# Performance work log

Measured on AMD Instinct MI355X. Metric: run time of the kernel, lower is better.

## Reference

```python
import jax, jax.numpy as jnp
import numpy as np

B, T, D, H = 8, 1024, 1024, 16
HD = D // H
SCALE = HD ** -0.5


def setup_inputs() -> dict:
    key = jax.random.key(0)
    ks = jax.random.split(key, 5)
    s = 0.02
    return {
        "hidden_states": jax.random.normal(ks[0], (B, T, D), jnp.float32),
        "Wq": jax.random.normal(ks[1], (D, D), jnp.float32) * s,
        "bq": jnp.zeros((D,), jnp.float32),
        "Wk": jax.random.normal(ks[2], (D, D), jnp.float32) * s,
        "bk": jnp.zeros((D,), jnp.float32),
        "Wv": jax.random.normal(ks[3], (D, D), jnp.float32) * s,
        "bv": jnp.zeros((D,), jnp.float32),
        "Wo": jax.random.normal(ks[4], (D, D), jnp.float32) * s,
        "bo": jnp.zeros((D,), jnp.float32),
    }


def _split_heads(x):
    # [B, T, D] -> [B, H, T, HD]
    return x.reshape(B, T, H, HD).transpose(0, 2, 1, 3)


def reference(hidden_states, Wq, bq, Wk, bk, Wv, bv, Wo, bo):
    q = _split_heads((hidden_states @ Wq + bq) * SCALE)
    k = _split_heads(hidden_states @ Wk + bk)
    v = _split_heads(hidden_states @ Wv + bv)
    # [B, H, T, T] attention scores
    scores = jnp.einsum("bhqd,bhkd->bhqk", q, k)
    probs = jax.nn.softmax(scores, axis=-1)
    attn = jnp.einsum("bhqk,bhkd->bhqd", probs, v)
    attn = attn.transpose(0, 2, 1, 3).reshape(B, T, D)
    return attn @ Wo + bo
```

## Files before the change

kernel.cpp:

```cpp
#include <hip/hip_runtime.h>

typedef unsigned short u16;
typedef __attribute__((ext_vector_type(4))) float f32x4;
typedef __attribute__((ext_vector_type(8))) __bf16 bf16x8;
typedef __attribute__((ext_vector_type(4))) __bf16 bf16x4;
typedef __attribute__((ext_vector_type(4))) unsigned short u16x4;
typedef __attribute__((ext_vector_type(8))) unsigned short u16x8;

static __device__ __forceinline__ u16 f2bf(float f) {
    union { float f; unsigned u; } v; v.f = f;
    unsigned r = v.u + 0x7FFFu + ((v.u >> 16) & 1u);
    return (u16)(r >> 16);
}

static __device__ __forceinline__ float exp2f_fast(float x) {
    float r; asm("v_exp_f32 %0, %1" : "=v"(r) : "v"(x)); return r;
}

static __device__ __forceinline__ void gload16(const u16* g, u16* l) {
    __builtin_amdgcn_global_load_lds(
        (const __attribute__((address_space(1))) unsigned int*)g,
        (__attribute__((address_space(3))) unsigned int*)l, 16, 0, 0);
}

template<int N> static __device__ __forceinline__ void vm_wait() {
    if constexpr (N == 3)      asm volatile("s_waitcnt vmcnt(3)" ::: "memory");
    else if constexpr (N == 2) asm volatile("s_waitcnt vmcnt(2)" ::: "memory");
    else                       asm volatile("s_waitcnt vmcnt(0)" ::: "memory");
}

#define SWZ64(row, ec) (((row) * 64) + ((((ec) ^ ((row) & 7))) << 3))

__global__ __launch_bounds__(256) void k_prep(
    const float* __restrict__ hs, u16* __restrict__ Xb,
    const float* __restrict__ W0, const float* __restrict__ W1,
    const float* __restrict__ W2, const float* __restrict__ W3,
    u16* __restrict__ T0, u16* __restrict__ T1, u16* __restrict__ T2, u16* __restrict__ T3,
    float s0) {
    __shared__ float tile[32][33];
    const int id = blockIdx.x;
    const int tid = threadIdx.x;
    if (id < 8192) {
        size_t i = (size_t)id * 256 + tid;
        float4 v = ((const float4*)hs)[i];
        u16x4 o; o[0] = f2bf(v.x); o[1] = f2bf(v.y); o[2] = f2bf(v.z); o[3] = f2bf(v.w);
        *(u16x4*)(Xb + i * 4) = o;
        return;
    }
    const int wid = id - 8192;
    const int z = wid >> 10, rem = wid & 1023;
    const int n0 = (rem & 31) * 32, k0 = (rem >> 5) * 32;
    const float* W; u16* Tt; float sc;
    switch (z) {
        case 0:  W = W0; Tt = T0; sc = s0;  break;
        case 1:  W = W1; Tt = T1; sc = 1.f; break;
        case 2:  W = W2; Tt = T2; sc = 1.f; break;
        default: W = W3; Tt = T3; sc = 1.f; break;
    }
    int r = tid >> 3, c = (tid & 7) * 4;
    float4 v = *(const float4*)(W + (size_t)(k0 + r) * 1024 + n0 + c);
    tile[r][c] = v.x; tile[r][c + 1] = v.y; tile[r][c + 2] = v.z; tile[r][c + 3] = v.w;
    __syncthreads();
    u16x4 o;
    o[0] = f2bf(tile[c][r] * sc);
    o[1] = f2bf(tile[c + 1][r] * sc);
    o[2] = f2bf(tile[c + 2][r] * sc);
    o[3] = f2bf(tile[c + 3][r] * sc);
    *(u16x4*)(Tt + (size_t)(n0 + r) * 1024 + k0 + c) = o;
}

__global__ __launch_bounds__(512, 4) void k_g128(
    const u16* __restrict__ A, const u16* __restrict__ Bt,
    const float* __restrict__ bias, const float* __restrict__ biasK, float qscale,
    u16* __restrict__ obf, u16* __restrict__ obK, float* __restrict__ of32,
    int ldc, int bias_row, int nblk, int cpx, int mode) {
    constexpr int ASLOT = 256 * 32;
    constexpr int BSLOT = 128 * 32;
    __shared__ u16 As[3 * ASLOT];
    __shared__ u16 Bs[3 * BSLOT];
    const int tid = threadIdx.x;
    const int l = tid & 63, w = tid >> 6;
    const int mw = w >> 1, nw = w & 1;
    const int fr = l & 15, gg = l >> 4, f4 = gg * 4;
    const int id = blockIdx.x;
    const int swz = (id & 7) * cpx + (id >> 3);
    const int bm = swz / nblk, bn = swz % nblk;
    const size_t m0 = (size_t)bm * 256, n0v = (size_t)bn * 128;

    const int srow = w * 16 + (l >> 2);
    const int schk = ((l & 3) ^ ((l >> 3) & 3)) * 8;
    const u16* agp0 = A + (m0 + srow) * 1024 + schk;
    const u16* agp1 = A + (m0 + 128 + srow) * 1024 + schk;
    const u16* bgp0 = Bt + (n0v + srow) * 1024 + schk;
    const int ldst = w * 512 + l * 8;

    const int fchk = (gg ^ ((fr >> 1) & 3)) * 8;
    int aoff[4], boff[4];
#pragma unroll
    for (int mt = 0; mt < 4; ++mt) aoff[mt] = (mw * 64 + mt * 16 + fr) * 32 + fchk;
#pragma unroll
    for (int nt = 0; nt < 4; ++nt) boff[nt] = (nw * 64 + nt * 16 + fr) * 32 + fchk;

    f32x4 acc[4][4] = {};

#define GSTG(S, J)                                                              \
    gload16(agp0 + (size_t)(J) * 32, As + (S) * ASLOT + ldst);                  \
    gload16(agp1 + (size_t)(J) * 32, As + (S) * ASLOT + 4096 + ldst);           \
    gload16(bgp0 + (size_t)(J) * 32, Bs + (S) * BSLOT + ldst);
    GSTG(0, 0) GSTG(1, 1)

#define TILE(S, SD, J, VMN, STG)                                                \
    {                                                                           \
        vm_wait<VMN>();                                                         \
        __builtin_amdgcn_s_barrier();                                           \
        bf16x8 afr[4], bfr[4];                                                  \
        _Pragma("unroll")                                                       \
        for (int nt = 0; nt < 4; ++nt)                                          \
            bfr[nt] = *(const bf16x8*)(&Bs[(S) * BSLOT + boff[nt]]);            \
        _Pragma("unroll")                                                       \
        for (int mt = 0; mt < 4; ++mt)                                          \
            afr[mt] = *(const bf16x8*)(&As[(S) * ASLOT + aoff[mt]]);            \
        if (STG) { GSTG(SD, (J) + 2) }                                          \
        __builtin_amdgcn_s_barrier();                                           \
        asm volatile("s_waitcnt lgkmcnt(0)" ::: "memory");                      \
        __builtin_amdgcn_sched_barrier(0);                                      \
        __builtin_amdgcn_s_setprio(1);                                          \
        _Pragma("unroll")                                                       \
        for (int mt = 0; mt < 4; ++mt)                                          \
            _Pragma("unroll")                                                   \
            for (int nt = 0; nt < 4; ++nt)                                      \
                acc[mt][nt] = __builtin_amdgcn_mfma_f32_16x16x32_bf16(afr[mt], bfr[nt], acc[mt][nt], 0, 0, 0); \
        __builtin_amdgcn_s_setprio(0);                                          \
    }

#pragma unroll 1
    for (int jb = 0; jb < 30; jb += 3) {
        TILE(0, 2, jb + 0, 3, true)
        TILE(1, 0, jb + 1, 3, true)
        TILE(2, 1, jb + 2, 3, true)
    }
    TILE(0, 2, 30, 3, false)
    TILE(1, 0, 31, 0, false)
#undef TILE
#undef GSTG

    const int mrow0 = (int)m0 + mw * 64;
    const int ncol0 = (int)n0v + nw * 64;
    if (mode == 1) {
#pragma unroll
        for (int mt = 0; mt < 4; ++mt)
#pragma unroll
            for (int nt = 0; nt < 4; ++nt) {
                const int col = ncol0 + nt * 16 + fr;
                const int seg = col >> 10, colm = col & 1023;
                const float bb = (seg ? biasK[colm] : bias[colm] * qscale);
                u16* op = seg ? obK : obf;
#pragma unroll
                for (int r = 0; r < 4; ++r)
                    op[(size_t)(mrow0 + mt * 16 + f4 + r) * 1024 + colm] = f2bf(acc[mt][nt][r] + bb);
            }
    } else if (mode == 2) {
#pragma unroll
        for (int mt = 0; mt < 4; ++mt) {
            float rb_[4];
#pragma unroll
            for (int r = 0; r < 4; ++r) rb_[r] = bias[mrow0 + mt * 16 + f4 + r];
#pragma unroll
            for (int nt = 0; nt < 4; ++nt) {
                const int col = ncol0 + nt * 16 + fr;
                const int colp = (col & ~31) | (((col >> 2) & 3) << 3) |
                                 (((col >> 4) & 1) << 2) | (col & 3);
#pragma unroll
                for (int r = 0; r < 4; ++r) {
                    const size_t row = (size_t)(mrow0 + mt * 16 + f4 + r);
                    obf[row * (size_t)ldc + colp] = f2bf(acc[mt][nt][r] + rb_[r]);
                }
            }
        }
    } else {
#pragma unroll
        for (int mt = 0; mt < 4; ++mt) {
            float rb_[4];
#pragma unroll
            for (int r = 0; r < 4; ++r)
                rb_[r] = bias_row ? bias[mrow0 + mt * 16 + f4 + r] : 0.f;
#pragma unroll
            for (int nt = 0; nt < 4; ++nt) {
                const int col = ncol0 + nt * 16 + fr;
                const float cb = bias_row ? 0.f : bias[col];
#pragma unroll
                for (int r = 0; r < 4; ++r) {
                    const size_t row = (size_t)(mrow0 + mt * 16 + f4 + r);
                    const float vv = acc[mt][nt][r] + cb + rb_[r];
                    if (of32) of32[row * (size_t)ldc + col] = vv;
                    else      obf[row * (size_t)ldc + col] = f2bf(vv);
                }
            }
        }
    }
}

static __device__ __forceinline__ void qk_tile(const u16* Ks, int fr, int gg,
                                               bf16x8 qA0, bf16x8 qA1, bf16x8 qB0, bf16x8 qB1,
                                               float mA, float mB, f32x4 sA[4], f32x4 sB[4]) {
    __builtin_amdgcn_s_setprio(1);
#pragma unroll
    for (int nt = 0; nt < 4; ++nt) {
        const int rk = nt * 16 + fr;
        const bf16x8 kf0 = *(const bf16x8*)(&Ks[SWZ64(rk, gg)]);
        const bf16x8 kf1 = *(const bf16x8*)(&Ks[SWZ64(rk, gg + 4)]);
        f32x4 z = {-mA, -mA, -mA, -mA};
        z = __builtin_amdgcn_mfma_f32_16x16x32_bf16(kf0, qA0, z, 0, 0, 0);
        z = __builtin_amdgcn_mfma_f32_16x16x32_bf16(kf1, qA1, z, 0, 0, 0);
        sA[nt] = z;
        f32x4 y = {-mB, -mB, -mB, -mB};
        y = __builtin_amdgcn_mfma_f32_16x16x32_bf16(kf0, qB0, y, 0, 0, 0);
        y = __builtin_amdgcn_mfma_f32_16x16x32_bf16(kf1, qB1, y, 0, 0, 0);
        sB[nt] = y;
    }
    __builtin_amdgcn_s_setprio(0);
}

static __device__ __forceinline__ void sm_tile(const f32x4 s[4], f32x4 o[4],
                                               float& m, float& lsum, bf16x4 p[4]) {
    float mymax = s[0][0];
#pragma unroll
    for (int nt = 0; nt < 4; ++nt)
#pragma unroll
        for (int r = 0; r < 4; ++r) mymax = fmaxf(mymax, s[nt][r]);
    float psn[4] = {0.f, 0.f, 0.f, 0.f};
#pragma unroll
    for (int nt = 0; nt < 4; ++nt)
#pragma unroll
        for (int r = 0; r < 4; ++r) {
            const float pp = exp2f_fast(s[nt][r]);
            psn[nt] += pp; p[nt][r] = (__bf16)pp;
        }
    float ps = (psn[0] + psn[1]) + (psn[2] + psn[3]);
    if (__builtin_expect(__any(mymax > 11.0f), 0)) {
        float rm = fmaxf(mymax, __shfl_xor(mymax, 16, 64));
        rm = fmaxf(rm, __shfl_xor(rm, 32, 64));
        const float d = fmaxf(rm, 0.f);
        const float fac = exp2f_fast(-d);
        m += d; lsum *= fac;
#pragma unroll
        for (int mt = 0; mt < 4; ++mt)
#pragma unroll
            for (int r = 0; r < 4; ++r) o[mt][r] *= fac;
        ps = 0.f;
#pragma unroll
        for (int nt = 0; nt < 4; ++nt)
#pragma unroll
            for (int r = 0; r < 4; ++r) {
                const float pp = exp2f_fast(s[nt][r] - d);
                ps += pp; p[nt][r] = (__bf16)pp;
            }
    }
    lsum += ps;
}

static __device__ __forceinline__ void pv_tile(const u16* Vs, int fr, int gg,
                                               const bf16x4 pA[4], const bf16x4 pB[4],
                                               f32x4 oA[4], f32x4 oB[4]) {
    const bf16x8 BA0 = __builtin_shufflevector(pA[0], pA[1], 0, 1, 2, 3, 4, 5, 6, 7);
    const bf16x8 BA1 = __builtin_shufflevector(pA[2], pA[3], 0, 1, 2, 3, 4, 5, 6, 7);
    const bf16x8 BB0 = __builtin_shufflevector(pB[0], pB[1], 0, 1, 2, 3, 4, 5, 6, 7);
    const bf16x8 BB1 = __builtin_shufflevector(pB[2], pB[3], 0, 1, 2, 3, 4, 5, 6, 7);
    __builtin_amdgcn_s_setprio(1);
#pragma unroll
    for (int mt = 0; mt < 4; ++mt) {
        const int rv = mt * 16 + fr;
        const bf16x8 vk0 = *(const bf16x8*)(&Vs[SWZ64(rv, gg)]);
        const bf16x8 vk1 = *(const bf16x8*)(&Vs[SWZ64(rv, gg + 4)]);
        oA[mt] = __builtin_amdgcn_mfma_f32_16x16x32_bf16(vk0, BA0, oA[mt], 0, 0, 0);
        oA[mt] = __builtin_amdgcn_mfma_f32_16x16x32_bf16(vk1, BA1, oA[mt], 0, 0, 0);
        oB[mt] = __builtin_amdgcn_mfma_f32_16x16x32_bf16(vk0, BB0, oB[mt], 0, 0, 0);
        oB[mt] = __builtin_amdgcn_mfma_f32_16x16x32_bf16(vk1, BB1, oB[mt], 0, 0, 0);
    }
    __builtin_amdgcn_s_setprio(0);
}

__global__ __launch_bounds__(256, 4) void k_flash(const u16* __restrict__ Q, const u16* __restrict__ K,
                                                  const u16* __restrict__ Vt2, u16* __restrict__ O) {
    __shared__ u16 Ks[2][64 * 64];
    __shared__ u16 Vs[3][64 * 64];
    const int tid = threadIdx.x;
    const int l = tid & 63, w = tid >> 6;
    const int id = blockIdx.x;
    const int swz = (id & 7) * 128 + (id >> 3);
    const int bh = swz >> 3, qt = swz & 7;
    const int b = bh >> 4, h = bh & 15;
    const int qw = qt * 128 + w * 32;
    const int fr = l & 15, gg = l >> 4, f4 = gg * 4, f8 = gg * 8;

    const u16* qpA = Q + ((size_t)(b * 1024 + qw + fr)) * 1024 + h * 64 + f8;
    const u16* qpB = qpA + 16 * 1024;
    const bf16x8 qA0 = *(const bf16x8*)qpA;
    const bf16x8 qA1 = *(const bf16x8*)(qpA + 32);
    const bf16x8 qB0 = *(const bf16x8*)qpB;
    const bf16x8 qB1 = *(const bf16x8*)(qpB + 32);

    const int jj0 = w * 2, jj1 = w * 2 + 1;
    const int sr0 = jj0 * 8 + (l >> 3), sr1 = jj1 * 8 + (l >> 3);
    const int sc = ((l & 7) ^ (l >> 3)) * 8;
    const u16* kg0 = K + ((size_t)(b * 1024 + sr0)) * 1024 + h * 64 + sc;
    const u16* kg1 = K + ((size_t)(b * 1024 + sr1)) * 1024 + h * 64 + sc;
    const u16* vg0 = Vt2 + ((size_t)(h * 64 + sr0)) * 8192 + b * 1024 + sc;
    const u16* vg1 = Vt2 + ((size_t)(h * 64 + sr1)) * 8192 + b * 1024 + sc;
    const int lk0 = jj0 * 512 + l * 8, lk1 = jj1 * 512 + l * 8;

#define FSTGK(S, kt)                                        \
    gload16(kg0 + (size_t)(kt) * 1024, Ks[S] + lk0);        \
    gload16(kg1 + (size_t)(kt) * 1024, Ks[S] + lk1);
#define FSTGV(S, kt)                                        \
    gload16(vg0 + (kt), Vs[S] + lk0);                       \
    gload16(vg1 + (kt), Vs[S] + lk1);

    f32x4 oA[4] = {}, oB[4] = {};
    float mA = 0.f, lA = 0.f, mB = 0.f, lB = 0.f;
    bf16x4 p0A[4], p0B[4], p1A[4], p1B[4];

    FSTGK(0, 0) FSTGV(0, 0)

#define FITER(T, QS, PS, KS, VS, PCA, PCB, PPA, PPB, DOPV, DOSTG)            \
    {                                                                        \
        vm_wait<2>();                                                        \
        __builtin_amdgcn_s_barrier();                                        \
        f32x4 sA[4], sB[4];                                                  \
        qk_tile(Ks[QS], fr, gg, qA0, qA1, qB0, qB1, mA, mB, sA, sB);         \
        if (DOSTG) { FSTGK(KS, ((T) + 1) * 64) FSTGV(VS, ((T) + 1) * 64) }   \
        if (DOPV) pv_tile(Vs[PS], fr, gg, PPA, PPB, oA, oB);                 \
        sm_tile(sA, oA, mA, lA, PCA);                                        \
        sm_tile(sB, oB, mB, lB, PCB);                                        \
    }

    FITER(0,  0, 0, 1, 1, p0A, p0B, p1A, p1B, 0, 1)
    FITER(1,  1, 0, 0, 2, p1A, p1B, p0A, p0B, 1, 1)
    FITER(2,  0, 1, 1, 0, p0A, p0B, p1A, p1B, 1, 1)
    FITER(3,  1, 2, 0, 1, p1A, p1B, p0A, p0B, 1, 1)
    FITER(4,  0, 0, 1, 2, p0A, p0B, p1A, p1B, 1, 1)
    FITER(5,  1, 1, 0, 0, p1A, p1B, p0A, p0B, 1, 1)
    FITER(6,  0, 2, 1, 1, p0A, p0B, p1A, p1B, 1, 1)
    FITER(7,  1, 0, 0, 2, p1A, p1B, p0A, p0B, 1, 1)
    FITER(8,  0, 1, 1, 0, p0A, p0B, p1A, p1B, 1, 1)
    FITER(9,  1, 2, 0, 1, p1A, p1B, p0A, p0B, 1, 1)
    FITER(10, 0, 0, 1, 2, p0A, p0B, p1A, p1B, 1, 1)
    FITER(11, 1, 1, 0, 0, p1A, p1B, p0A, p0B, 1, 1)
    FITER(12, 0, 2, 1, 1, p0A, p0B, p1A, p1B, 1, 1)
    FITER(13, 1, 0, 0, 2, p1A, p1B, p0A, p0B, 1, 1)
    FITER(14, 0, 1, 1, 0, p0A, p0B, p1A, p1B, 1, 1)
    FITER(15, 1, 2, 0, 0, p1A, p1B, p0A, p0B, 1, 0)
#undef FITER
    vm_wait<0>();
    __builtin_amdgcn_s_barrier();
    pv_tile(Vs[0], fr, gg, p1A, p1B, oA, oB);
#undef FSTGK
#undef FSTGV

    lA += __shfl_xor(lA, 16, 64); lA += __shfl_xor(lA, 32, 64);
    lB += __shfl_xor(lB, 16, 64); lB += __shfl_xor(lB, 32, 64);
    const float ivA = 1.0f / lA, ivB = 1.0f / lB;
    u16* opA = O + ((size_t)(b * 1024 + qw + fr)) * 1024 + h * 64;
    u16* opB = opA + 16 * 1024;
#pragma unroll
    for (int mt = 0; mt < 4; ++mt) {
        u16x4 oa, ob;
#pragma unroll
        for (int r = 0; r < 4; ++r) { oa[r] = f2bf(oA[mt][r] * ivA); ob[r] = f2bf(oB[mt][r] * ivB); }
        *(u16x4*)(opA + mt * 16 + f4) = oa;
        *(u16x4*)(opB + mt * 16 + f4) = ob;
    }
}

extern "C" void kernel_launch(void* const* d_in, const int* in_sizes, int n_in,
                              void* d_out, int out_size, void* d_ws, size_t ws_size,
                              hipStream_t stream) {
    (void)in_sizes; (void)n_in; (void)out_size; (void)ws_size;
    const float* hs = (const float*)d_in[0];
    const float* Wq = (const float*)d_in[1];
    const float* bq = (const float*)d_in[2];
    const float* Wk = (const float*)d_in[3];
    const float* bk = (const float*)d_in[4];
    const float* Wv = (const float*)d_in[5];
    const float* bv = (const float*)d_in[6];
    const float* Wo = (const float*)d_in[7];
    const float* bo = (const float*)d_in[8];
    float* out = (float*)d_out;
    char* ws = (char*)d_ws;
    const size_t MB = 1024ull * 1024ull;
    u16* Xb  = (u16*)(ws);
    u16* Wqt = (u16*)(ws + 16 * MB);
    u16* Wkt = (u16*)(ws + 18 * MB);
    u16* Wvt = (u16*)(ws + 20 * MB);
    u16* Wot = (u16*)(ws + 22 * MB);
    u16* Qb  = (u16*)(ws + 24 * MB);
    u16* Kb  = (u16*)(ws + 40 * MB);
    u16* Vt2 = (u16*)(ws + 56 * MB);
    u16* Ob  = Xb;

    const float SCALE_Q = 0.125f * 1.4426950408889634f;

    k_prep<<<dim3(12288), dim3(256), 0, stream>>>(hs, Xb, Wq, Wk, Wv, Wo,
                                                  Wqt, Wkt, Wvt, Wot, SCALE_Q);
    k_g128<<<dim3(512), dim3(512), 0, stream>>>(Xb, Wqt, bq, bk, SCALE_Q,
                                                Qb, Kb, nullptr, 1024, 0, 16, 64, 1);
    k_g128<<<dim3(256), dim3(512), 0, stream>>>(Wvt, Xb, bv, nullptr, 1.f,
                                                Vt2, nullptr, nullptr, 8192, 1, 64, 32, 2);
    k_flash<<<dim3(1024), dim3(256), 0, stream>>>(Qb, Kb, Vt2, Ob);
    k_g128<<<dim3(256), dim3(512), 0, stream>>>(Ob, Wot, bo, nullptr, 1.f,
                                                nullptr, nullptr, out, 1024, 0, 8, 32, 0);
}
```

Before: 156.8 us.

## Add dedicated 256x256-tile QK projection GEMM with 4-stage pipeline

Replaces the generic 256x128 GEMM for the fused Q/K projection with a specialised kernel using 256x256 block tiles, a 4-deep LDS ring and split A/B prefetch interleaved with two MFMA halves. The larger tile doubles operand reuse per block and halves the grid to 256 blocks, reducing global/LDS traffic per FLOP. Launch bounds on the remaining GEMM and the flash kernel are lowered from 4 to 2 waves-per-SIMD hints, which loosens register limits. The cost is higher LDS use (128KB per block), fewer resident blocks, and 256 blocks on a 256-CU part, which could leave tail imbalance.

```diff
diff --git a/kernel.cpp b/kernel.cpp
--- a/kernel.cpp
+++ b/kernel.cpp
@@ -24,7 +24,10 @@
 }
 
 template<int N> static __device__ __forceinline__ void vm_wait() {
-    if constexpr (N == 3)      asm volatile("s_waitcnt vmcnt(3)" ::: "memory");
+    if constexpr (N >= 8)      asm volatile("s_waitcnt vmcnt(8)" ::: "memory");
+    else if constexpr (N == 6) asm volatile("s_waitcnt vmcnt(6)" ::: "memory");
+    else if constexpr (N == 4) asm volatile("s_waitcnt vmcnt(4)" ::: "memory");
+    else if constexpr (N == 3) asm volatile("s_waitcnt vmcnt(3)" ::: "memory");
     else if constexpr (N == 2) asm volatile("s_waitcnt vmcnt(2)" ::: "memory");
     else                       asm volatile("s_waitcnt vmcnt(0)" ::: "memory");
 }
@@ -69,10 +72,124 @@
     *(u16x4*)(Tt + (size_t)(n0 + r) * 1024 + k0 + c) = o;
 }
 
-__global__ __launch_bounds__(512, 4) void k_g128(
+__global__ __launch_bounds__(512, 2) void k_gQK(
     const u16* __restrict__ A, const u16* __restrict__ Bt,
-    const float* __restrict__ bias, const float* __restrict__ biasK, float qscale,
-    u16* __restrict__ obf, u16* __restrict__ obK, float* __restrict__ of32,
+    const float* __restrict__ bq, const float* __restrict__ bk, float qscale,
+    u16* __restrict__ Qb, u16* __restrict__ Kb) {
+    constexpr int ASLOT = 256 * 32;
+    constexpr int BSLOT = 256 * 32;
+    __shared__ u16 As[4 * ASLOT];
+    __shared__ u16 Bs[4 * BSLOT];
+    const int tid = threadIdx.x;
+    const int l = tid & 63, w = tid >> 6;
+    const int mw = w >> 2, nw = w & 3;
+    const int fr = l & 15, gg = l >> 4, f4 = gg * 4;
+    const int id = blockIdx.x;
+    const int swz = (id & 7) * 32 + (id >> 3);
+    const int bm = swz >> 3, bn = swz & 7;
+    const size_t m0 = (size_t)bm * 256, n0v = (size_t)bn * 256;
+
+    const int srow = w * 16 + (l >> 2);
+    const int schk = ((l & 3) ^ ((l >> 3) & 3)) * 8;
+    const u16* agp0 = A + (m0 + srow) * 1024 + schk;
+    const u16* agp1 = A + (m0 + 128 + srow) * 1024 + schk;
+    const u16* bgp0 = Bt + (n0v + srow) * 1024 + schk;
+    const u16* bgp1 = Bt + (n0v + 128 + srow) * 1024 + schk;
+    const int ldst = w * 512 + l * 8;
+
+    const int fchk = (gg ^ ((fr >> 1) & 3)) * 8;
+    int aoff[8], boff[4];
+#pragma unroll
+    for (int mt = 0; mt < 8; ++mt) aoff[mt] = (mw * 128 + mt * 16 + fr) * 32 + fchk;
+#pragma unroll
+    for (int nt = 0; nt < 4; ++nt) boff[nt] = (nw * 64 + nt * 16 + fr) * 32 + fchk;
+
+    f32x4 acc[8][4] = {};
+
+#define PSTG(S, J)                                                              \
+    gload16(agp0 + (size_t)(J) * 32, As + (S) * ASLOT + ldst);                  \
+    gload16(agp1 + (size_t)(J) * 32, As + (S) * ASLOT + 4096 + ldst);           \
+    gload16(bgp0 + (size_t)(J) * 32, Bs + (S) * BSLOT + ldst);                  \
+    gload16(bgp1 + (size_t)(J) * 32, Bs + (S) * BSLOT + 4096 + ldst);
+    PSTG(0, 0) PSTG(1, 1) PSTG(2, 2)
+#undef PSTG
+
+#define TILE(S, J, VMN, STG)                                                    \
+    {                                                                           \
+        vm_wait<VMN>();                                                         \
+        __builtin_amdgcn_s_barrier();                                           \
+        bf16x8 afr[4], bfr[4];                                                  \
+        _Pragma("unroll")                                                       \
+        for (int nt = 0; nt < 4; ++nt)                                          \
+            bfr[nt] = *(const bf16x8*)(&Bs[(S) * BSLOT + boff[nt]]);            \
+        _Pragma("unroll")                                                       \
+        for (int mt = 0; mt < 4; ++mt)                                          \
+            afr[mt] = *(const bf16x8*)(&As[(S) * ASLOT + aoff[mt]]);            \
+        if (STG) {                                                              \
+            gload16(agp0 + (size_t)((J) + 3) * 32, As + (((S) + 3) & 3) * ASLOT + ldst);        \
+            gload16(agp1 + (size_t)((J) + 3) * 32, As + (((S) + 3) & 3) * ASLOT + 4096 + ldst); \
+        }                                                                       \
+        __builtin_amdgcn_s_barrier();                                           \
+        asm volatile("s_waitcnt lgkmcnt(0)" ::: "memory");                      \
+        __builtin_amdgcn_sched_barrier(0);                                      \
+        __builtin_amdgcn_s_setprio(1);                                          \
+        _Pragma("unroll")                                                       \
+        for (int mt = 0; mt < 4; ++mt)                                          \
+            _Pragma("unroll")                                                   \
+            for (int nt = 0; nt < 4; ++nt)                                      \
+                acc[mt][nt] = __builtin_amdgcn_mfma_f32_16x16x32_bf16(afr[mt], bfr[nt], acc[mt][nt], 0, 0, 0); \
+        __builtin_amdgcn_s_setprio(0);                                          \
+        _Pragma("unroll")                                                       \
+        for (int mt = 0; mt < 4; ++mt)                                          \
+            afr[mt] = *(const bf16x8*)(&As[(S) * ASLOT + aoff[4 + mt]]);        \
+        if (STG) {                                                              \
+            gload16(bgp0 + (size_t)((J) + 3) * 32, Bs + (((S) + 3) & 3) * BSLOT + ldst);        \
+            gload16(bgp1 + (size_t)((J) + 3) * 32, Bs + (((S) + 3) & 3) * BSLOT + 4096 + ldst); \
+        }                                                                       \
+        __builtin_amdgcn_s_barrier();                                           \
+        asm volatile("s_waitcnt lgkmcnt(0)" ::: "memory");                      \
+        __builtin_amdgcn_sched_barrier(0);                                      \
+        __builtin_amdgcn_s_setprio(1);                                          \
+        _Pragma("unroll")                                                       \
+        for (int mt = 0; mt < 4; ++mt)                                          \
+            _Pragma("unroll")                                                   \
+            for (int nt = 0; nt < 4; ++nt)                                      \
+                acc[4 + mt][nt] = __builtin_amdgcn_mfma_f32_16x16x32_bf16(afr[mt], bfr[nt], acc[4 + mt][nt], 0, 0, 0); \
+        __builtin_amdgcn_s_setprio(0);                                          \
+    }
+
+#pragma unroll 1
+    for (int jb = 0; jb < 28; jb += 4) {
+        TILE(0, jb + 0, 8, true)
+        TILE(1, jb + 1, 8, true)
+        TILE(2, jb + 2, 8, true)
+        TILE(3, jb + 3, 8, true)
+    }
+    TILE(0, 28, 8, true)
+    TILE(1, 29, 8, false)
+    TILE(2, 30, 4, false)
+    TILE(3, 31, 0, false)
+#undef TILE
+
+    const int mrow0 = (int)m0 + mw * 128;
+    const int ncol0 = (int)n0v + nw * 64;
+#pragma unroll
+    for (int mt = 0; mt < 8; ++mt)
+#pragma unroll
+        for (int nt = 0; nt < 4; ++nt) {
+            const int col = ncol0 + nt * 16 + fr;
+            const int seg = col >> 10, colm = col & 1023;
+            const float bb = (seg ? bk[colm] : bq[colm] * qscale);
+            u16* op = seg ? Kb : Qb;
+#pragma unroll
+            for (int r = 0; r < 4; ++r)
+                op[(size_t)(mrow0 + mt * 16 + f4 + r) * 1024 + colm] = f2bf(acc[mt][nt][r] + bb);
+        }
+}
+
+__global__ __launch_bounds__(512, 2) void k_g128(
+    const u16* __restrict__ A, const u16* __restrict__ Bt,
+    const float* __restrict__ bias, u16* __restrict__ obf, float* __restrict__ of32,
     int ldc, int bias_row, int nblk, int cpx, int mode) {
     constexpr int ASLOT = 256 * 32;
     constexpr int BSLOT = 128 * 32;
@@ -146,20 +263,7 @@
 
     const int mrow0 = (int)m0 + mw * 64;
     const int ncol0 = (int)n0v + nw * 64;
-    if (mode == 1) {
-#pragma unroll
-        for (int mt = 0; mt < 4; ++mt)
-#pragma unroll
-            for (int nt = 0; nt < 4; ++nt) {
-                const int col = ncol0 + nt * 16 + fr;
-                const int seg = col >> 10, colm = col & 1023;
-                const float bb = (seg ? biasK[colm] : bias[colm] * qscale);
-                u16* op = seg ? obK : obf;
-#pragma unroll
-                for (int r = 0; r < 4; ++r)
-                    op[(size_t)(mrow0 + mt * 16 + f4 + r) * 1024 + colm] = f2bf(acc[mt][nt][r] + bb);
-            }
-    } else if (mode == 2) {
+    if (mode == 2) {
 #pragma unroll
         for (int mt = 0; mt < 4; ++mt) {
             float rb_[4];
@@ -280,7 +384,7 @@
     __builtin_amdgcn_s_setprio(0);
 }
 
-__global__ __launch_bounds__(256, 4) void k_flash(const u16* __restrict__ Q, const u16* __restrict__ K,
+__global__ __launch_bounds__(256, 2) void k_flash(const u16* __restrict__ Q, const u16* __restrict__ K,
                                                   const u16* __restrict__ Vt2, u16* __restrict__ O) {
     __shared__ u16 Ks[2][64 * 64];
     __shared__ u16 Vs[3][64 * 64];
@@ -402,11 +506,8 @@
 
     k_prep<<<dim3(12288), dim3(256), 0, stream>>>(hs, Xb, Wq, Wk, Wv, Wo,
                                                   Wqt, Wkt, Wvt, Wot, SCALE_Q);
-    k_g128<<<dim3(512), dim3(512), 0, stream>>>(Xb, Wqt, bq, bk, SCALE_Q,
-                                                Qb, Kb, nullptr, 1024, 0, 16, 64, 1);
-    k_g128<<<dim3(256), dim3(512), 0, stream>>>(Wvt, Xb, bv, nullptr, 1.f,
-                                                Vt2, nullptr, nullptr, 8192, 1, 64, 32, 2);
+    k_gQK<<<dim3(256), dim3(512), 0, stream>>>(Xb, Wqt, bq, bk, SCALE_Q, Qb, Kb);
+    k_g128<<<dim3(256), dim3(512), 0, stream>>>(Wvt, Xb, bv, Vt2, nullptr, 8192, 1, 64, 32, 2);
     k_flash<<<dim3(1024), dim3(256), 0, stream>>>(Qb, Kb, Vt2, Ob);
-    k_g128<<<dim3(256), dim3(512), 0, stream>>>(Ob, Wot, bo, nullptr, 1.f,
-                                                nullptr, nullptr, out, 1024, 0, 8, 32, 0);
-}
+    k_g128<<<dim3(256), dim3(512), 0, stream>>>(Ob, Wot, bo, nullptr, out, 1024, 0, 8, 32, 0);
+}
```

Result: faster. 150.7 us (-3.9%).
